# Optimization experiments

Measured on AMD Instinct MI355X. Metric: run time of the kernel, lower is better.

## Reference

```python
import jax, jax.numpy as jnp
import numpy as np

N = 8192          # total neurons (n)
IN_NEURONS = 1024 # input_neurons
OUT_NEURONS = 256 # output_neurons


def setup_inputs() -> dict:
    key = jax.random.key(0)
    k1, k2 = jax.random.split(key)
    x = jax.random.normal(k1, (1, IN_NEURONS), dtype=jnp.float32)
    # learned adjacency weight (original uses kaiming_uniform; scale kept small for stability)
    W = jax.random.normal(k2, (N, N), dtype=jnp.float32) * 0.01
    return {"x": x, "W": W, "num_steps": 4}


def reference(x, W, num_steps):
    n = W.shape[0]
    # load_input_neurons: state = (W.T * pad(x[0], n)).T  ==  W * s0[:, None]
    s0 = jnp.pad(x[0], (0, n - x.shape[1]))        # [n]
    state = W * s0[:, None]                        # [n, n]

    # step(): next = sum_i(W.T * state[i]) then .T  ==  W * colsum(state)[:, None]
    def body(state, _):
        col_sum = state.sum(axis=0)                # [n]
        return W * col_sum[:, None], None

    state, _ = jax.lax.scan(body, state, None, length=num_steps)

    # extract_output_neurons: diagonal entries state[-i, -i], i = OUT..1
    return jnp.diagonal(state)[-OUT_NEURONS:]      # [OUT_NEURONS]
```

## Files before the change

### kernel.cpp

```cpp
#include <hip/hip_runtime.h>


namespace {
constexpr int N = 8192;
constexpr int NF4 = N / 4;
constexpr int IN_N = 1024;
constexpr int OUT_N = 256;
constexpr int BT = 256;

constexpr int B1 = 256;
constexpr int R1R = IN_N / B1;
constexpr int B2 = 1024;
constexpr int R2R = N / B2;

constexpr size_t OFF_V1 = 0;
constexpr size_t OFF_V2 = 8192;
constexpr size_t OFF_V3 = 16384;
constexpr size_t OFF_V4 = 24576;
constexpr size_t OFF_P  = 32768;

typedef float f4 __attribute__((ext_vector_type(4)));
}

__global__ void zero_vecs(float* __restrict__ ws) {
  int i = blockIdx.x * blockDim.x + threadIdx.x;
  if (i < 3 * N + OUT_N) ws[i] = 0.0f;
}

template <int ROWS>
__global__ __launch_bounds__(BT) void gemv_slab(const float* __restrict__ W,
                                                const float* __restrict__ vin,
                                                float* __restrict__ P) {
  __shared__ float sv[ROWS];
  const int b = blockIdx.x, t = threadIdx.x;
  const int i0 = b * ROWS;
  if (t < ROWS) sv[t] = vin[i0 + t];
  __syncthreads();
  const f4* __restrict__ W4 = reinterpret_cast<const f4*>(W);
  f4 acc[8];
#pragma unroll
  for (int k = 0; k < 8; ++k) acc[k] = (f4)(0.f);
#pragma unroll 2
  for (int i = 0; i < ROWS; ++i) {
    const float s = sv[i];
    const f4* __restrict__ row = W4 + (size_t)(i0 + i) * NF4;
#pragma unroll
    for (int k = 0; k < 8; ++k) {
      const f4 w = __builtin_nontemporal_load(row + k * BT + t);
      acc[k] += w * s;
    }
  }
  f4* __restrict__ P4 = reinterpret_cast<f4*>(P) + (size_t)b * NF4;
#pragma unroll
  for (int k = 0; k < 8; ++k) P4[k * BT + t] = acc[k];
}

template <int CS>
__global__ __launch_bounds__(BT) void reduce_cols(const float* __restrict__ P,
                                                  float* __restrict__ v) {
  const int j = blockIdx.x * BT + threadIdx.x;
  const int c0 = blockIdx.y * CS;
  float a = 0.f;
#pragma unroll 8
  for (int c = 0; c < CS; ++c) a += P[(size_t)(c0 + c) * N + j];
  atomicAdd(v + j, a);
}

__global__ __launch_bounds__(64) void gemv_tail(const float* __restrict__ W,
                                                const float* __restrict__ v3,
                                                float* __restrict__ v4) {
  __shared__ float sv[32];
  const int b = blockIdx.x, t = threadIdx.x;
  const int i0 = b * 32;
  if (t < 32) sv[t] = v3[i0 + t];
  __syncthreads();
  const f4* __restrict__ W4 = reinterpret_cast<const f4*>(W);
  f4 a = (f4)(0.f);
#pragma unroll 4
  for (int i = 0; i < 32; ++i) {
    const f4 w = W4[(size_t)(i0 + i) * NF4 + 1984 + t];
    a += w * sv[i];
  }
  atomicAdd(v4 + 4 * t + 0, a.x);
  atomicAdd(v4 + 4 * t + 1, a.y);
  atomicAdd(v4 + 4 * t + 2, a.z);
  atomicAdd(v4 + 4 * t + 3, a.w);
}

__global__ void diag_scale(const float* __restrict__ W,
                           const float* __restrict__ v4,
                           float* __restrict__ out) {
  const int t = threadIdx.x;
  const size_t j = (size_t)(N - OUT_N + t);
  out[t] = W[j * (N + 1)] * v4[t];
}

extern "C" void kernel_launch(void* const* d_in, const int* in_sizes, int n_in,
                              void* d_out, int out_size, void* d_ws, size_t ws_size,
                              hipStream_t stream) {
  const float* x = (const float*)d_in[0];
  const float* W = (const float*)d_in[1];
  float* ws = (float*)d_ws;
  float* v1 = ws + OFF_V1;
  float* v2 = ws + OFF_V2;
  float* v3 = ws + OFF_V3;
  float* v4 = ws + OFF_V4;
  float* P  = ws + OFF_P;
  float* out = (float*)d_out;

  zero_vecs<<<(3 * N + OUT_N + 255) / 256, 256, 0, stream>>>(ws);

  gemv_slab<R1R><<<B1, BT, 0, stream>>>(W, x, P);
  reduce_cols<32><<<dim3(N / BT, B1 / 32), BT, 0, stream>>>(P, v1);

  gemv_slab<R2R><<<B2, BT, 0, stream>>>(W, v1, P);
  reduce_cols<32><<<dim3(N / BT, B2 / 32), BT, 0, stream>>>(P, v2);

  gemv_slab<R2R><<<B2, BT, 0, stream>>>(W, v2, P);
  reduce_cols<32><<<dim3(N / BT, B2 / 32), BT, 0, stream>>>(P, v3);

  gemv_tail<<<N / 32, 64, 0, stream>>>(W, v3, v4);

  diag_scale<<<1, OUT_N, 0, stream>>>(W, v4, out);
}
```

Measured before the change: 444.5 us.

## Retile GEMV slabs into column tiles with taller row slabs

Each GEMV block now handles one of eight column tiles over a taller row slab (32 or 128 rows) instead of a full row over a few rows. This cuts the partial-sum buffer written and re-read by the column reduction from 1024 rows to 64, lowering extra memory traffic. Each thread keeps one accumulator and streams down rows, which trades per-block memory parallelism for longer dependency chains per thread. The reduction depth changes to 16 to match.

```diff
diff --git a/kernel.cpp b/kernel.cpp
--- a/kernel.cpp
+++ b/kernel.cpp
@@ -8,10 +8,11 @@
 constexpr int OUT_N = 256;
 constexpr int BT = 256;
 
-constexpr int B1 = 256;
-constexpr int R1R = IN_N / B1;
-constexpr int B2 = 1024;
-constexpr int R2R = N / B2;
+constexpr int NCT = 8;
+constexpr int R1R = 32;
+constexpr int R2R = 128;
+constexpr int SL1 = IN_N / R1R;
+constexpr int SL2 = N / R2R;
 
 constexpr size_t OFF_V1 = 0;
 constexpr size_t OFF_V2 = 8192;
@@ -33,26 +34,20 @@
                                                 float* __restrict__ P) {
   __shared__ float sv[ROWS];
   const int b = blockIdx.x, t = threadIdx.x;
-  const int i0 = b * ROWS;
-  if (t < ROWS) sv[t] = vin[i0 + t];
+  const int ct = b & (NCT - 1);
+  const int rs = b >> 3;
+  const int i0 = rs * ROWS;
+  for (int i = t; i < ROWS; i += BT) sv[i] = vin[i0 + i];
   __syncthreads();
   const f4* __restrict__ W4 = reinterpret_cast<const f4*>(W);
-  f4 acc[8];
-#pragma unroll
-  for (int k = 0; k < 8; ++k) acc[k] = (f4)(0.f);
-#pragma unroll 2
+  const int cf = ct * BT + t;
+  f4 acc = (f4)(0.f);
+#pragma unroll 8
   for (int i = 0; i < ROWS; ++i) {
-    const float s = sv[i];
-    const f4* __restrict__ row = W4 + (size_t)(i0 + i) * NF4;
-#pragma unroll
-    for (int k = 0; k < 8; ++k) {
-      const f4 w = __builtin_nontemporal_load(row + k * BT + t);
-      acc[k] += w * s;
-    }
+    const f4 w = __builtin_nontemporal_load(W4 + (size_t)(i0 + i) * NF4 + cf);
+    acc += w * sv[i];
   }
-  f4* __restrict__ P4 = reinterpret_cast<f4*>(P) + (size_t)b * NF4;
-#pragma unroll
-  for (int k = 0; k < 8; ++k) P4[k * BT + t] = acc[k];
+  reinterpret_cast<f4*>(P)[(size_t)rs * NF4 + cf] = acc;
 }
 
 template <int CS>
@@ -61,7 +56,7 @@
   const int j = blockIdx.x * BT + threadIdx.x;
   const int c0 = blockIdx.y * CS;
   float a = 0.f;
-#pragma unroll 8
+#pragma unroll
   for (int c = 0; c < CS; ++c) a += P[(size_t)(c0 + c) * N + j];
   atomicAdd(v + j, a);
 }
@@ -110,14 +105,14 @@
 
   zero_vecs<<<(3 * N + OUT_N + 255) / 256, 256, 0, stream>>>(ws);
 
-  gemv_slab<R1R><<<B1, BT, 0, stream>>>(W, x, P);
-  reduce_cols<32><<<dim3(N / BT, B1 / 32), BT, 0, stream>>>(P, v1);
+  gemv_slab<R1R><<<SL1 * NCT, BT, 0, stream>>>(W, x, P);
+  reduce_cols<16><<<dim3(N / BT, SL1 / 16), BT, 0, stream>>>(P, v1);
 
-  gemv_slab<R2R><<<B2, BT, 0, stream>>>(W, v1, P);
-  reduce_cols<32><<<dim3(N / BT, B2 / 32), BT, 0, stream>>>(P, v2);
+  gemv_slab<R2R><<<SL2 * NCT, BT, 0, stream>>>(W, v1, P);
+  reduce_cols<16><<<dim3(N / BT, SL2 / 16), BT, 0, stream>>>(P, v2);
 
-  gemv_slab<R2R><<<B2, BT, 0, stream>>>(W, v2, P);
-  reduce_cols<32><<<dim3(N / BT, B2 / 32), BT, 0, stream>>>(P, v3);
+  gemv_slab<R2R><<<SL2 * NCT, BT, 0, stream>>>(W, v2, P);
+  reduce_cols<16><<<dim3(N / BT, SL2 / 16), BT, 0, stream>>>(P, v3);
 
   gemv_tail<<<N / 32, 64, 0, stream>>>(W, v3, v4);
 
```

After: 435.4 us. 2.1% less time.
